# Optimization experiments

Hardware: AMD Instinct MI355X
Metric: run time of the kernel (lower is better)

Reference implementation:

```python
import jax, jax.numpy as jnp
import numpy as np

K = 512       # num_embeddings
D = 64        # dim_embeddings
BETA = 0.25   # commit_gain
GAMMA = 0.99  # EMA decay
EPS = 1e-05   # Laplace smoothing


def setup_inputs() -> dict:
    key = jax.random.key(0)
    k1, k2, k3 = jax.random.split(key, 3)
    enc_pred = jax.random.normal(k1, (32, D, 64, 64), dtype=jnp.float32)
    embeddings = jax.random.normal(k2, (K, D), dtype=jnp.float32)
    ema_m = jax.random.normal(k3, (K, D), dtype=jnp.float32)
    ema_M = jnp.zeros((K, 1), dtype=jnp.float32)
    return {"enc_pred": enc_pred, "embeddings": embeddings,
            "ema_m": ema_m, "ema_M": ema_M}


def reference(enc_pred, embeddings, ema_m, ema_M):
    B, _, H, W = enc_pred.shape
    x = jnp.transpose(enc_pred, (0, 2, 3, 1))          # [B, H, W, D]
    flat = x.reshape(-1, D)                            # [N, D], N = B*H*W

    # Squared L2 distances to all codewords: [N, K]
    dist = (jnp.sum(flat * flat, axis=1, keepdims=True)
            + jnp.sum(embeddings * embeddings, axis=1)
            - 2.0 * flat @ embeddings.T)
    idx = jnp.argmin(dist, axis=1)                     # [N]

    # Codebook lookup (equivalent to one-hot @ embeddings)
    quantized = embeddings[idx].reshape(x.shape)       # [B, H, W, D]

    # EMA codebook update (training branch, no_grad in torch)
    dm = jax.ops.segment_sum(flat, idx, num_segments=K)                 # [K, D]
    counts = jax.ops.segment_sum(jnp.ones((flat.shape[0], 1), flat.dtype),
                                 idx, num_segments=K)                   # [K, 1]
    new_m = GAMMA * ema_m + (1.0 - GAMMA) * dm
    new_M = GAMMA * ema_M + (1.0 - GAMMA) * counts
    N_tot = jnp.sum(new_M)
    new_M = (new_M + EPS) / (N_tot + EPS * K) * N_tot
    new_embeddings = new_m / new_M

    # Commitment loss (quantized detached)
    loss = BETA * jnp.mean((jax.lax.stop_gradient(quantized) - x) ** 2)

    # Straight-through estimator
    quant_ste = x + jax.lax.stop_gradient(quantized - x)
    out = jnp.transpose(quant_ste, (0, 3, 1, 2))       # [B, D, H, W]

    idx_ret = idx.reshape(B, H, W)[:, None, :, :]      # [B, 1, H, W]
    return (out, loss, idx_ret, new_embeddings, new_m, new_M)
```

## Files before the change

kernel.cpp:

```cpp
#include <hip/hip_runtime.h>

#define KCODES 512
#define DIM 64
#define NB 32
#define NH 64
#define NW 64
#define NPTS (NB*NH*NW)
#define HW (NH*NW)

#define O_OUT  0
#define O_LOSS 8388608
#define O_IDX  8388609
#define O_EMB  8519681
#define O_M    8552449
#define O_MM   8585217

#define W_DM   0
#define W_CNT  32768
#define W_LOSS 33280
#define W_SUMM 33281
#define W_C    33282
#define W_ZERO 33282

#define XPAD 68
#define EPAD 68

__global__ void cnorm_kernel(const float* __restrict__ emb,
                             const float* __restrict__ emaM,
                             float* __restrict__ ws) {
    int k = blockIdx.x * blockDim.x + threadIdx.x;
    if (k >= KCODES) return;
    float s = 0.f;
    #pragma unroll
    for (int d = 0; d < DIM; ++d) { float v = emb[k*DIM + d]; s += v*v; }
    ws[W_C + k] = s;
    float m = emaM[k];
    #pragma unroll
    for (int off = 32; off >= 1; off >>= 1) m += __shfl_down(m, off, 64);
    if ((k & 63) == 0) atomicAdd(&ws[W_SUMM], m);
}

__global__ __launch_bounds__(256, 2) void assign_kernel(
    const float* __restrict__ enc, const float* __restrict__ emb,
    float* __restrict__ out, float* __restrict__ ws)
{
    __shared__ float XL[128*XPAD];
    __shared__ float EL[128*EPAD];
    __shared__ float cnT[128];
    __shared__ int   bestI[128];

    const int t  = threadIdx.x;
    const int tx = t & 15;
    const int ty = t >> 4;
    const int wv = t >> 6, w = t & 63;
    const int R0 = blockIdx.x * 2;

    #pragma unroll
    for (int r2 = 0; r2 < 2; ++r2) {
        int R = R0 + r2, b = R >> 6, h = R & 63;
        const float* base = enc + (size_t)b*64*HW + (size_t)h*64 + w;
        int p = r2*64 + w;
        #pragma unroll
        for (int it = 0; it < 4; ++it) {
            int d0 = (it*4 + wv)*4;
            float4 v = make_float4(base[(size_t)(d0+0)*HW], base[(size_t)(d0+1)*HW],
                                   base[(size_t)(d0+2)*HW], base[(size_t)(d0+3)*HW]);
            *(float4*)(&XL[p*XPAD + d0]) = v;
        }
    }

    float best[8]; int bidx[8];
    #pragma unroll
    for (int i = 0; i < 8; ++i) { best[i] = 3.402823466e38f; bidx[i] = 0; }

    for (int tile = 0; tile < 4; ++tile) {
        __syncthreads();
        const float* esrc = emb + (size_t)tile*128*64;
        #pragma unroll
        for (int it = 0; it < 8; ++it) {
            int idx = t + it*256;
            *(float4*)(&EL[(idx >> 4)*EPAD + (idx & 15)*4]) =
                *(const float4*)(esrc + (idx >> 4)*64 + (idx & 15)*4);
        }
        if (t < 128) cnT[t] = ws[W_C + tile*128 + t];
        __syncthreads();

        float acc[8][8];
        #pragma unroll
        for (int i = 0; i < 8; ++i)
            #pragma unroll
            for (int j = 0; j < 8; ++j) acc[i][j] = 0.f;

        for (int c = 0; c < 16; ++c) {
            float4 xf[8], ef[8];
            #pragma unroll
            for (int i = 0; i < 8; ++i) {
                int p = 2*ty + (i&1) + 32*(i>>1);
                xf[i] = *(const float4*)(&XL[p*XPAD + c*4]);
            }
            #pragma unroll
            for (int j = 0; j < 8; ++j) {
                int r = tx + 16*j;
                ef[j] = *(const float4*)(&EL[r*EPAD + c*4]);
            }
            #pragma unroll
            for (int i = 0; i < 8; ++i)
                #pragma unroll
                for (int j = 0; j < 8; ++j) {
                    acc[i][j] = fmaf(xf[i].x, ef[j].x, acc[i][j]);
                    acc[i][j] = fmaf(xf[i].y, ef[j].y, acc[i][j]);
                    acc[i][j] = fmaf(xf[i].z, ef[j].z, acc[i][j]);
                    acc[i][j] = fmaf(xf[i].w, ef[j].w, acc[i][j]);
                }
        }

        #pragma unroll
        for (int j = 0; j < 8; ++j) {
            int k = tile*128 + tx + 16*j;
            float cn = cnT[tx + 16*j];
            #pragma unroll
            for (int i = 0; i < 8; ++i) {
                float s = cn - 2.f*acc[i][j];
                if (s < best[i]) { best[i] = s; bidx[i] = k; }
            }
        }
    }

    #pragma unroll
    for (int i = 0; i < 8; ++i) {
        float b = best[i]; int kx = bidx[i];
        #pragma unroll
        for (int off = 1; off < 16; off <<= 1) {
            float ob = __shfl_xor(b, off, 64);
            int   ok = __shfl_xor(kx, off, 64);
            if (ob < b || (ob == b && ok < kx)) { b = ob; kx = ok; }
        }
        if (tx == 0) bestI[2*ty + (i&1) + 32*(i>>1)] = kx;
    }
    __syncthreads();
    if (t < 128) out[O_IDX + (size_t)R0*64 + t] = (float)bestI[t];
}

__global__ __launch_bounds__(1024, 1) void scatter_kernel(
    const float* __restrict__ enc, const float* __restrict__ emb,
    float* __restrict__ out, float* __restrict__ ws)
{
    __shared__ float dmL[KCODES][DIM+1];
    __shared__ float cntL[KCODES];
    __shared__ float redL[16];

    const int t  = threadIdx.x;
    const int w  = t & 63;
    const int wv = t >> 6;
    const int rw = wv & 7;
    const int role = wv >> 3;
    const int pg = w >> 4, dl = w & 15;
    const int drot = (wv & 7) * 8;

    float* dmf = &dmL[0][0];
    for (int i = t; i < KCODES*(DIM+1); i += 1024) dmf[i] = 0.f;
    if (t < KCODES) cntL[t] = 0.f;
    __syncthreads();

    const int R = blockIdx.x * 8 + rw;
    const int b = R >> 6, h = R & 63;
    const float* base  = enc + (size_t)b*(64*HW) + (size_t)h*64;
    float*       obase = out + O_OUT + (size_t)b*(64*HW) + (size_t)h*64;

    const int bidx = (int)out[O_IDX + (size_t)R*64 + w];
    float lsum = 0.f;

    if (role == 0) {
        atomicAdd(&cntL[bidx], 1.0f);
        #pragma unroll
        for (int c = 0; c < 4; ++c) {
            #pragma unroll
            for (int jj = 0; jj < 16; ++jj) {
                int p  = jj*4 + pg;
                int kb = __shfl(bidx, p, 64);
                int d  = (c*16 + dl + drot) & 63;
                atomicAdd(&dmL[kb][d], base[(size_t)d*HW + p]);
            }
        }
    } else {
        #pragma unroll
        for (int c = 0; c < 4; ++c) {
            #pragma unroll
            for (int jj = 0; jj < 16; ++jj) {
                int p  = jj*4 + pg;
                int kb = __shfl(bidx, p, 64);
                int d  = (c*16 + dl + drot) & 63;
                float xv = base[(size_t)d*HW + p];
                float q  = emb[kb*64 + d];
                obase[(size_t)d*HW + p] = q;
                float df = q - xv;
                lsum = fmaf(df, df, lsum);
            }
        }
    }

    #pragma unroll
    for (int off = 32; off >= 1; off >>= 1) lsum += __shfl_down(lsum, off, 64);
    if (w == 0) redL[wv] = lsum;
    __syncthreads();
    if (t == 0) {
        float s = 0.f;
        #pragma unroll
        for (int v = 8; v < 16; ++v) s += redL[v];
        atomicAdd(&ws[W_LOSS], s);
    }

    for (int k = wv*32; k < wv*32 + 32; ++k) {
        float c = cntL[k];
        if (c == 0.f) continue;
        atomicAdd(&ws[W_DM + k*64 + w], dmL[k][w]);
        if (w == 0) atomicAdd(&ws[W_CNT + k], c);
    }
}

__global__ void finalize_kernel(const float* __restrict__ emam,
                                const float* __restrict__ emaM,
                                float* __restrict__ out,
                                const float* __restrict__ ws)
{
    int i = blockIdx.x * blockDim.x + threadIdx.x;
    int k = i >> 6;
    float Ntot = 0.99f * ws[W_SUMM] + 0.01f * (float)NPTS;
    float nM = 0.99f * emaM[k] + 0.01f * ws[W_CNT + k];
    float sm = (nM + 1e-5f) / (Ntot + 1e-5f * (float)KCODES) * Ntot;
    float nm = 0.99f * emam[i] + 0.01f * ws[W_DM + i];
    out[O_M + i] = nm;
    out[O_EMB + i] = nm / sm;
    if ((i & 63) == 0) out[O_MM + k] = sm;
    if (i == 0) out[O_LOSS] = 0.25f * ws[W_LOSS] / (float)((size_t)NPTS * DIM);
}

extern "C" void kernel_launch(void* const* d_in, const int* in_sizes, int n_in,
                              void* d_out, int out_size, void* d_ws, size_t ws_size,
                              hipStream_t stream)
{
    const float* enc  = (const float*)d_in[0];
    const float* emb  = (const float*)d_in[1];
    const float* emam = (const float*)d_in[2];
    const float* emaM = (const float*)d_in[3];
    float* out = (float*)d_out;
    float* ws  = (float*)d_ws;

    hipMemsetAsync(ws, 0, (size_t)W_ZERO * sizeof(float), stream);
    cnorm_kernel<<<2, 256, 0, stream>>>(emb, emaM, ws);
    assign_kernel<<<NPTS/128, 256, 0, stream>>>(enc, emb, out, ws);
    scatter_kernel<<<256, 1024, 0, stream>>>(enc, emb, out, ws);
    finalize_kernel<<<(KCODES*DIM)/256, 256, 0, stream>>>(emam, emaM, out, ws);
}
```

Before: 231.6 us.

## Halve scatter kernel shared histogram by processing dims in two phases

The scatter kernel's shared dm histogram shrinks from 512x65 to 512x33 floats. Dimensions are now handled in two phases of 32, with a flush to global atomics and a zeroing pass between them, so two 1024-thread blocks can fit per CU. Each block now covers 4 rows instead of 8 and the grid doubles to 512 blocks, with two waves per row splitting the 16-dim chunks. The cost is extra __syncthreads, twice as many global atomic flushes (each block covers fewer rows), and the loss of the per-wave dimension rotation that reduced LDS atomic contention.

Measured after the change: 253.6 us. +9.5%, slower.

```diff
diff --git a/kernel.cpp b/kernel.cpp
--- a/kernel.cpp
+++ b/kernel.cpp
@@ -141,28 +141,29 @@
     if (t < 128) out[O_IDX + (size_t)R0*64 + t] = (float)bestI[t];
 }
 
-__global__ __launch_bounds__(1024, 1) void scatter_kernel(
+__global__ __launch_bounds__(1024, 2) void scatter_kernel(
     const float* __restrict__ enc, const float* __restrict__ emb,
     float* __restrict__ out, float* __restrict__ ws)
 {
-    __shared__ float dmL[KCODES][DIM+1];
+    __shared__ float dmL[KCODES][33];
     __shared__ float cntL[KCODES];
     __shared__ float redL[16];
 
     const int t  = threadIdx.x;
     const int w  = t & 63;
     const int wv = t >> 6;
-    const int rw = wv & 7;
     const int role = wv >> 3;
+    const int rq = wv & 7;
+    const int rw = rq >> 1;
+    const int q  = rq & 1;
     const int pg = w >> 4, dl = w & 15;
-    const int drot = (wv & 7) * 8;
 
     float* dmf = &dmL[0][0];
-    for (int i = t; i < KCODES*(DIM+1); i += 1024) dmf[i] = 0.f;
+    for (int i = t; i < KCODES*33; i += 1024) dmf[i] = 0.f;
     if (t < KCODES) cntL[t] = 0.f;
     __syncthreads();
 
-    const int R = blockIdx.x * 8 + rw;
+    const int R = blockIdx.x * 4 + rw;
     const int b = R >> 6, h = R & 63;
     const float* base  = enc + (size_t)b*(64*HW) + (size_t)h*64;
     float*       obase = out + O_OUT + (size_t)b*(64*HW) + (size_t)h*64;
@@ -170,33 +171,43 @@
     const int bidx = (int)out[O_IDX + (size_t)R*64 + w];
     float lsum = 0.f;
 
-    if (role == 0) {
-        atomicAdd(&cntL[bidx], 1.0f);
-        #pragma unroll
-        for (int c = 0; c < 4; ++c) {
+    #pragma unroll
+    for (int phase = 0; phase < 2; ++phase) {
+        if (role == 0) {
+            if (phase == 0 && q == 0) atomicAdd(&cntL[bidx], 1.0f);
             #pragma unroll
             for (int jj = 0; jj < 16; ++jj) {
                 int p  = jj*4 + pg;
                 int kb = __shfl(bidx, p, 64);
-                int d  = (c*16 + dl + drot) & 63;
-                atomicAdd(&dmL[kb][d], base[(size_t)d*HW + p]);
-            }
-        }
-    } else {
-        #pragma unroll
-        for (int c = 0; c < 4; ++c) {
+                int d  = phase*32 + q*16 + dl;
+                atomicAdd(&dmL[kb][d & 31], base[(size_t)d*HW + p]);
+            }
+        } else {
             #pragma unroll
             for (int jj = 0; jj < 16; ++jj) {
                 int p  = jj*4 + pg;
                 int kb = __shfl(bidx, p, 64);
-                int d  = (c*16 + dl + drot) & 63;
+                int d  = phase*32 + q*16 + dl;
                 float xv = base[(size_t)d*HW + p];
-                float q  = emb[kb*64 + d];
-                obase[(size_t)d*HW + p] = q;
-                float df = q - xv;
+                float qv = emb[kb*64 + d];
+                obase[(size_t)d*HW + p] = qv;
+                float df = qv - xv;
                 lsum = fmaf(df, df, lsum);
             }
         }
+        __syncthreads();
+
+        for (int k = wv*32; k < wv*32 + 32; ++k) {
+            float c = cntL[k];
+            if (c == 0.f) continue;
+            if (w < 32) {
+                float v = dmL[k][w];
+                dmL[k][w] = 0.f;
+                atomicAdd(&ws[W_DM + k*64 + phase*32 + w], v);
+            }
+            if (phase == 1 && w == 0) atomicAdd(&ws[W_CNT + k], c);
+        }
+        __syncthreads();
     }
 
     #pragma unroll
@@ -208,13 +219,6 @@
         #pragma unroll
         for (int v = 8; v < 16; ++v) s += redL[v];
         atomicAdd(&ws[W_LOSS], s);
-    }
-
-    for (int k = wv*32; k < wv*32 + 32; ++k) {
-        float c = cntL[k];
-        if (c == 0.f) continue;
-        atomicAdd(&ws[W_DM + k*64 + w], dmL[k][w]);
-        if (w == 0) atomicAdd(&ws[W_CNT + k], c);
     }
 }
 
@@ -249,6 +253,6 @@
     hipMemsetAsync(ws, 0, (size_t)W_ZERO * sizeof(float), stream);
     cnorm_kernel<<<2, 256, 0, stream>>>(emb, emaM, ws);
     assign_kernel<<<NPTS/128, 256, 0, stream>>>(enc, emb, out, ws);
-    scatter_kernel<<<256, 1024, 0, stream>>>(enc, emb, out, ws);
+    scatter_kernel<<<512, 1024, 0, stream>>>(enc, emb, out, ws);
     finalize_kernel<<<(KCODES*DIM)/256, 256, 0, stream>>>(emam, emaM, out, ws);
 }
```

## Compute commitment loss algebraically from norms and per-code sums

Applied to the files above, without the earlier changes.

The per-element (q-x)^2 loss accumulation in the scatter kernel is replaced by an algebraic decomposition: sum|x|^2 is accumulated in the assign kernel from data already loaded, and sum(|e_k|^2*count_k - 2 e_k·dm_k) is computed from the per-code shared sums. This drops the re-read of the encoder input in the output-writing half of the scatter kernel. It adds global float atomics per wave in assign, and the loss may differ from a direct computation because of cancellation in float32.

After: 294.4 us. 1.27x slower.

```diff
diff --git a/kernel.cpp b/kernel.cpp
--- a/kernel.cpp
+++ b/kernel.cpp
@@ -17,10 +17,11 @@
 
 #define W_DM   0
 #define W_CNT  32768
-#define W_LOSS 33280
+#define W_XSQ  33280
 #define W_SUMM 33281
-#define W_C    33282
-#define W_ZERO 33282
+#define W_LSC  33282
+#define W_C    33284
+#define W_ZERO 33284
 
 #define XPAD 68
 #define EPAD 68
@@ -55,6 +56,7 @@
     const int wv = t >> 6, w = t & 63;
     const int R0 = blockIdx.x * 2;
 
+    float xsq = 0.f;
     #pragma unroll
     for (int r2 = 0; r2 < 2; ++r2) {
         int R = R0 + r2, b = R >> 6, h = R & 63;
@@ -66,8 +68,12 @@
             float4 v = make_float4(base[(size_t)(d0+0)*HW], base[(size_t)(d0+1)*HW],
                                    base[(size_t)(d0+2)*HW], base[(size_t)(d0+3)*HW]);
             *(float4*)(&XL[p*XPAD + d0]) = v;
-        }
-    }
+            xsq += v.x*v.x + v.y*v.y + v.z*v.z + v.w*v.w;
+        }
+    }
+    #pragma unroll
+    for (int off = 32; off >= 1; off >>= 1) xsq += __shfl_down(xsq, off, 64);
+    if (w == 0) atomicAdd(&ws[W_XSQ], xsq);
 
     float best[8]; int bidx[8];
     #pragma unroll
@@ -147,7 +153,6 @@
 {
     __shared__ float dmL[KCODES][DIM+1];
     __shared__ float cntL[KCODES];
-    __shared__ float redL[16];
 
     const int t  = threadIdx.x;
     const int w  = t & 63;
@@ -168,7 +173,6 @@
     float*       obase = out + O_OUT + (size_t)b*(64*HW) + (size_t)h*64;
 
     const int bidx = (int)out[O_IDX + (size_t)R*64 + w];
-    float lsum = 0.f;
 
     if (role == 0) {
         atomicAdd(&cntL[bidx], 1.0f);
@@ -190,32 +194,27 @@
                 int p  = jj*4 + pg;
                 int kb = __shfl(bidx, p, 64);
                 int d  = (c*16 + dl + drot) & 63;
-                float xv = base[(size_t)d*HW + p];
-                float q  = emb[kb*64 + d];
-                obase[(size_t)d*HW + p] = q;
-                float df = q - xv;
-                lsum = fmaf(df, df, lsum);
-            }
-        }
-    }
-
-    #pragma unroll
-    for (int off = 32; off >= 1; off >>= 1) lsum += __shfl_down(lsum, off, 64);
-    if (w == 0) redL[wv] = lsum;
+                obase[(size_t)d*HW + p] = emb[kb*64 + d];
+            }
+        }
+    }
     __syncthreads();
-    if (t == 0) {
-        float s = 0.f;
-        #pragma unroll
-        for (int v = 8; v < 16; ++v) s += redL[v];
-        atomicAdd(&ws[W_LOSS], s);
-    }
-
+
+    float lsc = 0.f;
     for (int k = wv*32; k < wv*32 + 32; ++k) {
         float c = cntL[k];
         if (c == 0.f) continue;
-        atomicAdd(&ws[W_DM + k*64 + w], dmL[k][w]);
-        if (w == 0) atomicAdd(&ws[W_CNT + k], c);
-    }
+        float v = dmL[k][w];
+        lsc = fmaf(-2.f*v, emb[k*64 + w], lsc);
+        atomicAdd(&ws[W_DM + k*64 + w], v);
+        if (w == 0) {
+            atomicAdd(&ws[W_CNT + k], c);
+            lsc = fmaf(c, ws[W_C + k], lsc);
+        }
+    }
+    #pragma unroll
+    for (int off = 32; off >= 1; off >>= 1) lsc += __shfl_down(lsc, off, 64);
+    if (w == 0 && lsc != 0.f) atomicAdd(&ws[W_LSC], lsc);
 }
 
 __global__ void finalize_kernel(const float* __restrict__ emam,
@@ -232,7 +231,8 @@
     out[O_M + i] = nm;
     out[O_EMB + i] = nm / sm;
     if ((i & 63) == 0) out[O_MM + k] = sm;
-    if (i == 0) out[O_LOSS] = 0.25f * ws[W_LOSS] / (float)((size_t)NPTS * DIM);
+    if (i == 0)
+        out[O_LOSS] = 0.25f * (ws[W_XSQ] + ws[W_LSC]) / (float)((size_t)NPTS * DIM);
 }
 
 extern "C" void kernel_launch(void* const* d_in, const int* in_sizes, int n_in,
```
